# Kernel tuning notes

Hardware: AMD Instinct MI355X
Metric: run time of the kernel (lower is better)

The kernel has to match this reference:

```python
import jax, jax.numpy as jnp
import numpy as np
from jax import lax

SQRT2 = 1.4142135623730951
NEG_SLOPE = 0.2


def _haar_kernels():
    l = np.ones((1, 2), np.float32) / np.float32(np.sqrt(2.0))
    h = l.copy()
    h[0, 0] = -h[0, 0]
    ll = l.T @ l
    lh = h.T @ l
    hl = l.T @ h
    hh = h.T @ h
    return (jnp.asarray(ll), jnp.asarray(lh), jnp.asarray(hl), jnp.asarray(hh))


def _blur_kernel():
    k = np.array([1.0, 3.0, 3.0, 1.0], np.float32)
    K = np.outer(k, k)
    K /= K.sum()
    return jnp.asarray(K)


def upfirdn2d(x, kernel, up=1, down=1, pad=(0, 0, 0, 0)):
    # x: [B,C,H,W]; depthwise FIR matching StyleGAN2 upfirdn2d semantics:
    # upsample by zero-insertion (up-1 zeros AFTER each sample), pad, true
    # convolution (kernel flipped, since lax does cross-correlation), then
    # stride-`down` decimation. Trailing zeros of torch's upsampling are
    # folded into the right/bottom pad (+up-1).
    B, C, H, W = x.shape
    px0, px1, py0, py1 = pad
    w = jnp.flip(kernel, (0, 1))[None, None].astype(x.dtype)  # [1,1,kh,kw]
    y = lax.conv_general_dilated(
        x.reshape(B * C, 1, H, W), w,
        window_strides=(down, down),
        padding=((py0, py1 + up - 1), (px0, px1 + up - 1)),
        lhs_dilation=(up, up),
        dimension_numbers=('NCHW', 'OIHW', 'NCHW'))
    return y.reshape(B, C, y.shape[2], y.shape[3])


def setup_inputs() -> dict:
    key = jax.random.key(0)
    k1, k2, k3 = jax.random.split(key, 3)
    x = jax.random.normal(k1, (8, 16, 512, 512), dtype=jnp.float32)
    conv_w = jax.random.normal(k2, (512, 16, 1, 1), dtype=jnp.float32)
    conv_b = jax.random.normal(k3, (512,), dtype=jnp.float32) * 0.1
    return {"x": x, "conv_w": conv_w, "conv_b": conv_b}


def reference(x, conv_w, conv_b):
    ll, lh, hl, hh = _haar_kernels()
    # ---- InverseHaarTransform(4): 16ch [B,16,H,W] -> 4ch [B,4,2H,2W] ----
    xll, xlh, xhl, xhh = jnp.split(x, 4, axis=1)
    p = (1, 0, 1, 0)
    inv = (upfirdn2d(xll, ll, up=2, pad=p)
           + upfirdn2d(xlh, -lh, up=2, pad=p)
           + upfirdn2d(xhl, -hl, up=2, pad=p)
           + upfirdn2d(xhh, hh, up=2, pad=p))
    # ---- Downsample(blur_kernel=[1,3,3,1]): [B,4,2H,2W] -> [B,4,H,W] ----
    bk = _blur_kernel()
    pp = bk.shape[0] - 2  # p = len(kernel) - factor
    pad0, pad1 = (pp + 1) // 2, pp // 2
    dwn = upfirdn2d(inv, bk, down=2, pad=(pad0, pad1, pad0, pad1))
    # ---- HaarTransform(4): [B,4,H,W] -> [B,16,H/2,W/2] ----
    new_in = jnp.concatenate(
        [upfirdn2d(dwn, k, down=2, pad=(0, 0, 0, 0)) for k in (ll, lh, hl, hh)],
        axis=1)
    # ---- ConvLayer: EqualConv2d 1x1 (no bias) + FusedLeakyReLU ----
    fan_in = conv_w.shape[1] * conv_w.shape[2] * conv_w.shape[3]
    scale = 1.0 / float(np.sqrt(fan_in))
    out = jnp.einsum('bchw,oc->bohw', new_in, conv_w[:, :, 0, 0] * scale)
    out = out + conv_b[None, :, None, None]
    out = jnp.where(out >= 0, out, NEG_SLOPE * out) * SQRT2
    return (new_in, out)
```

## Files before the change

kernel.cpp:

```cpp
#include <hip/hip_runtime.h>


#define H_IN 512
#define W_IN 512
#define H_OUT 256
#define W_OUT 256
#define NB 8
#define C_MID 16
#define C_OUT 512

typedef float fx4 __attribute__((ext_vector_type(4)));

__device__ __forceinline__ float cL(int fsel, float a0, float a1, float a2, float a3) {
  return fsel == 0 ? (a0 + 7.f*a1 + 7.f*a2 + a3) : (a0 + a1 - a2 - a3);
}
__device__ __forceinline__ float cH(int fsel, float a0, float a1, float a2, float a3) {
  return fsel == 0 ? (a0 + 5.f*a1 - 5.f*a2 - a3) : (a0 - a1 - a2 + a3);
}

__global__ __launch_bounds__(256) void k_stage1(const float* __restrict__ x,
                                                float* __restrict__ nin) {
  const int ox = threadIdx.x;
  const int by = blockIdx.x;
  const int bz = blockIdx.y;
  const int b = bz >> 2, ch = bz & 3;
  const int x0 = 2 * ox - 1;
  const int yb = 8 * by - 1;

  float acc[4][4];
#pragma unroll
  for (int i = 0; i < 4; ++i)
#pragma unroll
    for (int j = 0; j < 4; ++j) acc[i][j] = 0.f;

#pragma unroll
  for (int g = 0; g < 4; ++g) {
    const int gY = g & 1, gX = g >> 1;
    const float sg = (g == 1 || g == 2) ? -1.f : 1.f;
    const float* xp = x + (size_t)(b * 16 + g * 4 + ch) * (H_IN * W_IN);
    float uL[10], uH[10];
#pragma unroll
    for (int t = 0; t < 10; ++t) {
      const int yy = yb + t;
      float r0 = 0.f, r1 = 0.f, r2 = 0.f, r3 = 0.f;
      if (yy >= 0 && yy < H_IN) {
        const float* row = xp + (size_t)yy * W_IN;
        r0 = (x0 >= 0) ? row[x0] : 0.f;
        r1 = row[x0 + 1];
        r2 = row[x0 + 2];
        r3 = (x0 + 3 < W_IN) ? row[x0 + 3] : 0.f;
      }
      uL[t] = cL(gX, r0, r1, r2, r3);
      uH[t] = cH(gX, r0, r1, r2, r3);
    }
#pragma unroll
    for (int j = 0; j < 4; ++j) {
      const float l0 = uL[2*j], l1 = uL[2*j+1], l2 = uL[2*j+2], l3 = uL[2*j+3];
      const float h0 = uH[2*j], h1 = uH[2*j+1], h2 = uH[2*j+2], h3 = uH[2*j+3];
      acc[0][j] += sg * cL(gY, l0, l1, l2, l3);
      acc[1][j] += sg * cH(gY, l0, l1, l2, l3);
      acc[2][j] += sg * cL(gY, h0, h1, h2, h3);
      acc[3][j] += sg * cH(gY, h0, h1, h2, h3);
    }
  }

#pragma unroll
  for (int comp = 0; comp < 4; ++comp)
#pragma unroll
    for (int j = 0; j < 4; ++j) {
      const int oy = 4 * by + j;
      nin[((size_t)(b * 16 + comp * 4 + ch) * H_OUT + oy) * W_OUT + ox] =
          acc[comp][j] * (1.f / 256.f);
    }
}

__global__ __launch_bounds__(256) void k_stage2(const float* __restrict__ nin,
                                                const float* __restrict__ w,
                                                const float* __restrict__ bias,
                                                float* __restrict__ out) {
  __shared__ float ws[C_OUT * 16];
  __shared__ float bs[C_OUT];
  const int t = threadIdx.x;
#pragma unroll
  for (int i = 0; i < 32; ++i) ws[t + 256 * i] = w[t + 256 * i] * 0.25f;
  bs[t] = bias[t];
  bs[t + 256] = bias[t + 256];
  __syncthreads();

  const int by = blockIdx.x;
  const int b  = blockIdx.y;
  const int y  = 4 * by + (t >> 6);
  const int xq = (t & 63) * 4;

  const float* np = nin + ((size_t)(b * C_MID) * H_OUT + y) * W_OUT + xq;
  fx4 v[16];
#pragma unroll
  for (int c = 0; c < 16; ++c)
    v[c] = *reinterpret_cast<const fx4*>(np + (size_t)c * (H_OUT * W_OUT));

  float* op = out + ((size_t)(b * C_OUT) * H_OUT + y) * W_OUT + xq;
  const float s2 = 1.41421356237309515f;
#pragma unroll 2
  for (int o = 0; o < C_OUT; ++o) {
    const float* wr = &ws[o * 16];
    const float bo = bs[o];
    float ax = bo, ay = bo, az = bo, aw = bo;
#pragma unroll
    for (int c = 0; c < 16; ++c) {
      const float wc = wr[c];
      ax = fmaf(wc, v[c].x, ax);
      ay = fmaf(wc, v[c].y, ay);
      az = fmaf(wc, v[c].z, az);
      aw = fmaf(wc, v[c].w, aw);
    }
    ax = (ax >= 0.f ? ax : 0.2f * ax) * s2;
    ay = (ay >= 0.f ? ay : 0.2f * ay) * s2;
    az = (az >= 0.f ? az : 0.2f * az) * s2;
    aw = (aw >= 0.f ? aw : 0.2f * aw) * s2;
    fx4 r; r.x = ax; r.y = ay; r.z = az; r.w = aw;
    __builtin_nontemporal_store(r,
        reinterpret_cast<fx4*>(op + (size_t)o * (H_OUT * W_OUT)));
  }
}

extern "C" void kernel_launch(void* const* d_in, const int* in_sizes, int n_in,
                              void* d_out, int out_size, void* d_ws, size_t ws_size,
                              hipStream_t stream) {
  const float* x    = (const float*)d_in[0];
  const float* w    = (const float*)d_in[1];
  const float* bias = (const float*)d_in[2];
  float* nin = (float*)d_out;
  float* out = (float*)d_out + (size_t)NB * C_MID * H_OUT * W_OUT;

  k_stage1<<<dim3(64, 32), dim3(256), 0, stream>>>(x, nin);
  k_stage2<<<dim3(64, 8), dim3(256), 0, stream>>>(nin, w, bias, out);
}
```

Before: 264.8 us.

## Vectorize stage1 per-thread 4-wide outputs and split stage2 output channels across blocks

Stage1 now has each thread compute 4 adjacent output columns from 128-bit row loads. It reuses the overlapping horizontal taps and writes the result with float4 stores, with fewer blocks in the grid. Stage2 splits the 512 output channels into 4 chunks across blockIdx.z, which gives more blocks and a smaller shared weight footprint. It also reads the weights as float4 from LDS. The aim is better coalescing and fewer redundant loads in stage1, and more parallelism and occupancy in the store-bound stage2, at the cost of reloading the nin inputs 4 times.

```diff
diff --git a/kernel.cpp b/kernel.cpp
--- a/kernel.cpp
+++ b/kernel.cpp
@@ -20,71 +20,103 @@
 
 __global__ __launch_bounds__(256) void k_stage1(const float* __restrict__ x,
                                                 float* __restrict__ nin) {
-  const int ox = threadIdx.x;
-  const int by = blockIdx.x;
+  const int t  = threadIdx.x;
+  const int q  = t & 63;
+  const int rq = blockIdx.x * 4 + (t >> 6);
   const int bz = blockIdx.y;
   const int b = bz >> 2, ch = bz & 3;
-  const int x0 = 2 * ox - 1;
-  const int yb = 8 * by - 1;
+  const int yb = 8 * rq - 1;
 
-  float acc[4][4];
+  const float WL[2][4] = {{1.f, 7.f, 7.f, 1.f}, {1.f, 1.f, -1.f, -1.f}};
+  const float WH[2][4] = {{1.f, 5.f, -5.f, -1.f}, {1.f, -1.f, -1.f, 1.f}};
+
+  float acc[4][4][4];
 #pragma unroll
   for (int i = 0; i < 4; ++i)
 #pragma unroll
-    for (int j = 0; j < 4; ++j) acc[i][j] = 0.f;
+    for (int j = 0; j < 4; ++j)
+#pragma unroll
+      for (int k = 0; k < 4; ++k) acc[i][j][k] = 0.f;
 
 #pragma unroll
   for (int g = 0; g < 4; ++g) {
     const int gY = g & 1, gX = g >> 1;
     const float sg = (g == 1 || g == 2) ? -1.f : 1.f;
     const float* xp = x + (size_t)(b * 16 + g * 4 + ch) * (H_IN * W_IN);
-    float uL[10], uH[10];
 #pragma unroll
-    for (int t = 0; t < 10; ++t) {
-      const int yy = yb + t;
-      float r0 = 0.f, r1 = 0.f, r2 = 0.f, r3 = 0.f;
-      if (yy >= 0 && yy < H_IN) {
-        const float* row = xp + (size_t)yy * W_IN;
-        r0 = (x0 >= 0) ? row[x0] : 0.f;
-        r1 = row[x0 + 1];
-        r2 = row[x0 + 2];
-        r3 = (x0 + 3 < W_IN) ? row[x0 + 3] : 0.f;
+    for (int tt = 0; tt < 10; ++tt) {
+      const int yy = yb + tt;
+      if (yy < 0 || yy >= H_IN) continue;
+      const float* row = xp + (size_t)yy * W_IN + 8 * q;
+      float c[12];
+      c[0] = (q > 0) ? row[-1] : 0.f;
+      const fx4 m0 = *reinterpret_cast<const fx4*>(row);
+      const fx4 m1 = *reinterpret_cast<const fx4*>(row + 4);
+      c[1] = m0.x; c[2] = m0.y; c[3] = m0.z; c[4] = m0.w;
+      c[5] = m1.x; c[6] = m1.y; c[7] = m1.z; c[8] = m1.w;
+      if (q < 63) {
+        const fx4 m2 = *reinterpret_cast<const fx4*>(row + 8);
+        c[9] = m2.x; c[10] = m2.y; c[11] = m2.z;
+      } else {
+        c[9] = 0.f; c[10] = 0.f; c[11] = 0.f;
       }
-      uL[t] = cL(gX, r0, r1, r2, r3);
-      uH[t] = cH(gX, r0, r1, r2, r3);
-    }
+      float vL[4], vH[4];
 #pragma unroll
-    for (int j = 0; j < 4; ++j) {
-      const float l0 = uL[2*j], l1 = uL[2*j+1], l2 = uL[2*j+2], l3 = uL[2*j+3];
-      const float h0 = uH[2*j], h1 = uH[2*j+1], h2 = uH[2*j+2], h3 = uH[2*j+3];
-      acc[0][j] += sg * cL(gY, l0, l1, l2, l3);
-      acc[1][j] += sg * cH(gY, l0, l1, l2, l3);
-      acc[2][j] += sg * cL(gY, h0, h1, h2, h3);
-      acc[3][j] += sg * cH(gY, h0, h1, h2, h3);
+      for (int xo = 0; xo < 4; ++xo) {
+        const float a0 = c[2*xo], a1 = c[2*xo+1], a2 = c[2*xo+2], a3 = c[2*xo+3];
+        vL[xo] = cL(gX, a0, a1, a2, a3);
+        vH[xo] = cH(gX, a0, a1, a2, a3);
+      }
+#pragma unroll
+      for (int j = 0; j < 4; ++j) {
+        const int p = tt - 2 * j;
+        if (p < 0 || p > 3) continue;
+        const float wl = sg * WL[gY][p];
+        const float wh = sg * WH[gY][p];
+#pragma unroll
+        for (int xo = 0; xo < 4; ++xo) {
+          acc[0][j][xo] = fmaf(wl, vL[xo], acc[0][j][xo]);
+          acc[1][j][xo] = fmaf(wh, vL[xo], acc[1][j][xo]);
+          acc[2][j][xo] = fmaf(wl, vH[xo], acc[2][j][xo]);
+          acc[3][j][xo] = fmaf(wh, vH[xo], acc[3][j][xo]);
+        }
+      }
     }
   }
 
+  const float inv = 1.f / 256.f;
 #pragma unroll
   for (int comp = 0; comp < 4; ++comp)
 #pragma unroll
     for (int j = 0; j < 4; ++j) {
-      const int oy = 4 * by + j;
-      nin[((size_t)(b * 16 + comp * 4 + ch) * H_OUT + oy) * W_OUT + ox] =
-          acc[comp][j] * (1.f / 256.f);
+      fx4 r;
+      r.x = acc[comp][j][0] * inv; r.y = acc[comp][j][1] * inv;
+      r.z = acc[comp][j][2] * inv; r.w = acc[comp][j][3] * inv;
+      *reinterpret_cast<fx4*>(
+          nin + ((size_t)(b * 16 + comp * 4 + ch) * H_OUT + 4 * rq + j) * W_OUT + 4 * q) = r;
     }
+}
+
+__device__ __forceinline__ fx4 vfma(fx4 v, float s, fx4 a) {
+  a.x = fmaf(v.x, s, a.x); a.y = fmaf(v.y, s, a.y);
+  a.z = fmaf(v.z, s, a.z); a.w = fmaf(v.w, s, a.w);
+  return a;
 }
 
 __global__ __launch_bounds__(256) void k_stage2(const float* __restrict__ nin,
                                                 const float* __restrict__ w,
                                                 const float* __restrict__ bias,
                                                 float* __restrict__ out) {
-  __shared__ float ws[C_OUT * 16];
-  __shared__ float bs[C_OUT];
+  __shared__ fx4 ws4[128 * 4];
+  __shared__ float bs[128];
   const int t = threadIdx.x;
-#pragma unroll
-  for (int i = 0; i < 32; ++i) ws[t + 256 * i] = w[t + 256 * i] * 0.25f;
-  bs[t] = bias[t];
-  bs[t + 256] = bias[t + 256];
+  const int chunk = blockIdx.z;
+  const int obase = 128 * chunk;
+
+  const fx4* w4 = reinterpret_cast<const fx4*>(w + (size_t)obase * 16);
+  ws4[t]       = w4[t] * 0.25f;
+  ws4[t + 256] = w4[t + 256] * 0.25f;
+  if (t < 128) bs[t] = bias[obase + t];
   __syncthreads();
 
   const int by = blockIdx.x;
@@ -98,27 +130,26 @@
   for (int c = 0; c < 16; ++c)
     v[c] = *reinterpret_cast<const fx4*>(np + (size_t)c * (H_OUT * W_OUT));
 
-  float* op = out + ((size_t)(b * C_OUT) * H_OUT + y) * W_OUT + xq;
+  float* op = out + ((size_t)(b * C_OUT + obase) * H_OUT + y) * W_OUT + xq;
   const float s2 = 1.41421356237309515f;
 #pragma unroll 2
-  for (int o = 0; o < C_OUT; ++o) {
-    const float* wr = &ws[o * 16];
+  for (int o = 0; o < 128; ++o) {
+    const fx4 w0 = ws4[4*o], w1 = ws4[4*o+1], w2 = ws4[4*o+2], w3 = ws4[4*o+3];
     const float bo = bs[o];
-    float ax = bo, ay = bo, az = bo, aw = bo;
-#pragma unroll
-    for (int c = 0; c < 16; ++c) {
-      const float wc = wr[c];
-      ax = fmaf(wc, v[c].x, ax);
-      ay = fmaf(wc, v[c].y, ay);
-      az = fmaf(wc, v[c].z, az);
-      aw = fmaf(wc, v[c].w, aw);
-    }
-    ax = (ax >= 0.f ? ax : 0.2f * ax) * s2;
-    ay = (ay >= 0.f ? ay : 0.2f * ay) * s2;
-    az = (az >= 0.f ? az : 0.2f * az) * s2;
-    aw = (aw >= 0.f ? aw : 0.2f * aw) * s2;
-    fx4 r; r.x = ax; r.y = ay; r.z = az; r.w = aw;
-    __builtin_nontemporal_store(r,
+    fx4 a; a.x = bo; a.y = bo; a.z = bo; a.w = bo;
+    a = vfma(v[0],  w0.x, a); a = vfma(v[1],  w0.y, a);
+    a = vfma(v[2],  w0.z, a); a = vfma(v[3],  w0.w, a);
+    a = vfma(v[4],  w1.x, a); a = vfma(v[5],  w1.y, a);
+    a = vfma(v[6],  w1.z, a); a = vfma(v[7],  w1.w, a);
+    a = vfma(v[8],  w2.x, a); a = vfma(v[9],  w2.y, a);
+    a = vfma(v[10], w2.z, a); a = vfma(v[11], w2.w, a);
+    a = vfma(v[12], w3.x, a); a = vfma(v[13], w3.y, a);
+    a = vfma(v[14], w3.z, a); a = vfma(v[15], w3.w, a);
+    a.x = (a.x >= 0.f ? a.x : 0.2f * a.x) * s2;
+    a.y = (a.y >= 0.f ? a.y : 0.2f * a.y) * s2;
+    a.z = (a.z >= 0.f ? a.z : 0.2f * a.z) * s2;
+    a.w = (a.w >= 0.f ? a.w : 0.2f * a.w) * s2;
+    __builtin_nontemporal_store(a,
         reinterpret_cast<fx4*>(op + (size_t)o * (H_OUT * W_OUT)));
   }
 }
@@ -132,6 +163,6 @@
   float* nin = (float*)d_out;
   float* out = (float*)d_out + (size_t)NB * C_MID * H_OUT * W_OUT;
 
-  k_stage1<<<dim3(64, 32), dim3(256), 0, stream>>>(x, nin);
-  k_stage2<<<dim3(64, 8), dim3(256), 0, stream>>>(nin, w, bias, out);
+  k_stage1<<<dim3(16, 32), dim3(256), 0, stream>>>(x, nin);
+  k_stage2<<<dim3(64, 8, 4), dim3(256), 0, stream>>>(nin, w, bias, out);
 }
```

Result: faster. 257.4 us (-2.8%).
